# Kernel tuning notes

Measured on AMD Instinct MI355X. Metric: run time of the kernel, lower is better.

## Reference

```python
import jax, jax.numpy as jnp
import numpy as np

B, T, C, H = 4, 2048, 1024, 16
D = C // H  # head dim = 64

def setup_inputs() -> dict:
    key = jax.random.key(0)
    k1, k2, k3 = jax.random.split(key, 3)
    s = 1.0 / np.sqrt(C)
    return {
        "x": jax.random.normal(k1, (B, T, C), dtype=jnp.float32),
        "W_attn": jax.random.normal(k2, (C, 3 * C), dtype=jnp.float32) * s,
        "b_attn": jnp.zeros((3 * C,), dtype=jnp.float32),
        "W_proj": jax.random.normal(k3, (C, C), dtype=jnp.float32) * s,
        "b_proj": jnp.zeros((C,), dtype=jnp.float32),
    }

def reference(x, W_attn, b_attn, W_proj, b_proj):
    qkv = x @ W_attn + b_attn                      # [B,T,3C]
    q, k, v = jnp.split(qkv, 3, axis=-1)
    # [B,T,C] -> [B,H,T,D]
    q = q.reshape(B, T, H, D).transpose(0, 2, 1, 3)
    k = k.reshape(B, T, H, D).transpose(0, 2, 1, 3)
    v = v.reshape(B, T, H, D).transpose(0, 2, 1, 3)
    scale = 1.0 / np.sqrt(D)
    att = jnp.einsum('bhqd,bhkd->bhqk', q, k) * scale   # [B,H,T,T]
    causal = jnp.tril(jnp.ones((T, T), dtype=bool))
    att = jnp.where(causal[None, None], att, jnp.float32(-jnp.inf))
    att = jax.nn.softmax(att, axis=-1)
    y = jnp.einsum('bhqk,bhkd->bhqd', att, v)            # [B,H,T,D]
    y = y.transpose(0, 2, 1, 3).reshape(B, T, C)
    return y @ W_proj + b_proj
```

## Files before the change

kernel.cpp:

```cpp
#include <hip/hip_runtime.h>
#include <cstdint>
#include <cstddef>

typedef __bf16 bf16;
typedef __bf16 bf16x8 __attribute__((ext_vector_type(8)));
typedef __bf16 bf16x4 __attribute__((ext_vector_type(4)));
typedef short  s16x4  __attribute__((ext_vector_type(4)));
typedef float  f32x4  __attribute__((ext_vector_type(4)));

#define MFMA16(a, b, c) __builtin_amdgcn_mfma_f32_16x16x32_bf16((a), (b), (c), 0, 0, 0)

#if __has_builtin(__builtin_amdgcn_mfma_f32_16x16x16bf16_1k)
#define HAVE_K16 1
#else
#define HAVE_K16 0
#endif

#if __has_builtin(__builtin_amdgcn_exp2f)
#define EXP2(x) __builtin_amdgcn_exp2f(x)
#else
#define EXP2(x) exp2f(x)
#endif

constexpr int Bsz = 4;
constexpr int T   = 2048;
constexpr int Cd  = 1024;
constexpr int Hn  = 16;
constexpr int Mrows = Bsz * T;
constexpr int QKV_LD = 3 * Cd;

constexpr float QSCALE = 0.125f * 1.4426950408889634f;

__global__ __launch_bounds__(256) void prep(const float* __restrict__ x,
                                            const float* __restrict__ W_attn,
                                            const float* __restrict__ W_proj,
                                            bf16* __restrict__ xb,
                                            bf16* __restrict__ Wat,
                                            bf16* __restrict__ Wpt) {
    __shared__ float tile[32][33];
    const int bid = blockIdx.x;
    const int tid = threadIdx.x;
    if (bid < 4096) {
        const int i = (bid * 256 + tid) * 8;
        float4 a = *(const float4*)(x + i);
        float4 b = *(const float4*)(x + i + 4);
        bf16x8 o;
        o[0] = (bf16)a.x; o[1] = (bf16)a.y; o[2] = (bf16)a.z; o[3] = (bf16)a.w;
        o[4] = (bf16)b.x; o[5] = (bf16)b.y; o[6] = (bf16)b.z; o[7] = (bf16)b.w;
        *(bf16x8*)(xb + i) = o;
        return;
    }
    const float* W; bf16* Wt; int NDIM, bx, by;
    if (bid < 4096 + 3072) {
        const int r = bid - 4096;
        W = W_attn; Wt = Wat; NDIM = QKV_LD; bx = r % 96; by = r / 96;
    } else {
        const int r = bid - 7168;
        W = W_proj; Wt = Wpt; NDIM = Cd; bx = r & 31; by = r >> 5;
    }
    const int k0 = by * 32, n0 = bx * 32;
    const int tx = tid & 31, ty = tid >> 5;
    #pragma unroll
    for (int r = 0; r < 32; r += 8)
        tile[r + ty][tx] = W[(size_t)(k0 + r + ty) * NDIM + n0 + tx];
    __syncthreads();
    #pragma unroll
    for (int r = 0; r < 32; r += 8)
        Wt[(size_t)(n0 + r + ty) * Cd + k0 + tx] = (bf16)tile[tx][r + ty];
}

template <int N, bool OUT_BF16>
__global__ __launch_bounds__(512, 1) void gemm128x256(const bf16* __restrict__ A,
                                                      const bf16* __restrict__ Bt,
                                                      const float* __restrict__ bias,
                                                      void* __restrict__ outp,
                                                      float oscale, int oscale_n) {
    constexpr int K  = 1024;
    constexpr int KT = 16;
    __shared__ __align__(16) bf16 lds[73728];

    const int tid  = threadIdx.x;
    const int wv   = tid >> 6;
    const int lane = tid & 63;
    const int wm   = wv >> 2;
    const int wn   = wv & 3;
    const int quad = lane >> 4, c16 = lane & 15;
    const int sw   = c16 & 7;

    const int lin  = (int)blockIdx.x;
    const int mIdx = (lin & 7) + 8 * ((lin >> 3) & 7);
    const int nIdx = lin >> 6;
    const int m0   = mIdx * 128;
    const int n0   = nIdx * 256;

    auto stage = [&](int kt) {
        if (kt >= KT) return;
        const int db = kt % 3;
        #pragma unroll
        for (int r = 0; r < 2; ++r) {
            const int idx  = r * 512 + tid;
            const int slot = idx >> 3;
            const int kg   = kt * 64 + (((idx & 7) ^ (slot & 7)) << 3);
            __builtin_amdgcn_global_load_lds(
                (const __attribute__((address_space(1))) void*)(A + (size_t)(m0 + slot) * K + kg),
                (__attribute__((address_space(3))) void*)(&lds[db * 8192 + (r * 8 + wv) * 512]),
                16, 0, 0);
        }
        #pragma unroll
        for (int h = 0; h < 2; ++h)
            #pragma unroll
            for (int r = 0; r < 2; ++r) {
                const int idx  = r * 512 + tid;
                const int slot = idx >> 3;
                const int kg   = kt * 64 + (((idx & 7) ^ (slot & 7)) << 3);
                __builtin_amdgcn_global_load_lds(
                    (const __attribute__((address_space(1))) void*)(Bt + (size_t)(n0 + h * 128 + slot) * K + kg),
                    (__attribute__((address_space(3))) void*)(&lds[24576 + db * 16384 + h * 8192 + (r * 8 + wv) * 512]),
                    16, 0, 0);
            }
    };

    f32x4 acc[4][4] = {};
    bf16x8 af[4][2], bfv[4][2];

#define TILE_BODY(DB, SKT)                                                        \
    {                                                                             \
        _Pragma("unroll") for (int mq = 0; mq < 4; ++mq)                          \
            _Pragma("unroll") for (int ks = 0; ks < 2; ++ks)                      \
                af[mq][ks] = *(const bf16x8*)&lds[(DB) * 8192 +                   \
                    (wm * 64 + mq * 16 + c16) * 64 + (((ks * 4 + quad) ^ sw) << 3)]; \
        _Pragma("unroll") for (int nf = 0; nf < 4; ++nf)                          \
            _Pragma("unroll") for (int ks = 0; ks < 2; ++ks)                      \
                bfv[nf][ks] = *(const bf16x8*)&lds[24576 + (DB) * 16384 +         \
                    ((nf >> 1) * 128 + wn * 32 + (nf & 1) * 16 + c16) * 64 +      \
                    (((ks * 4 + quad) ^ sw) << 3)];                               \
        stage(SKT);                                                               \
        __builtin_amdgcn_s_setprio(1);                                            \
        _Pragma("unroll") for (int mq = 0; mq < 4; ++mq)                          \
            _Pragma("unroll") for (int nf = 0; nf < 4; ++nf)                      \
                _Pragma("unroll") for (int ks = 0; ks < 2; ++ks)                  \
                    acc[mq][nf] = MFMA16(af[mq][ks], bfv[nf][ks], acc[mq][nf]);   \
        __builtin_amdgcn_s_setprio(0);                                            \
    }
#define VMBAR(NSTR)                                                               \
    asm volatile("s_waitcnt vmcnt(" NSTR ")" ::: "memory");                       \
    __builtin_amdgcn_s_barrier();

    stage(0);
    stage(1);

    #pragma unroll 1
    for (int i = 0; i < 5; ++i) {
        const int u = 3 * i;
        VMBAR("6") TILE_BODY(0, u + 2)
        VMBAR("6") TILE_BODY(1, u + 3)
        VMBAR("6") TILE_BODY(2, u + 4)
    }
    VMBAR("0") TILE_BODY(0, KT)

#undef TILE_BODY
#undef VMBAR

    #pragma unroll
    for (int nf = 0; nf < 4; ++nf) {
        const int n = n0 + (nf >> 1) * 128 + wn * 32 + (nf & 1) * 16 + c16;
        const float bv = bias[n];
        const float sc = (n < oscale_n) ? oscale : 1.0f;
        #pragma unroll
        for (int mq = 0; mq < 4; ++mq) {
            const int rowb = m0 + wm * 64 + mq * 16 + quad * 4;
            #pragma unroll
            for (int r = 0; r < 4; ++r) {
                float val = (acc[mq][nf][r] + bv) * sc;
                if (OUT_BF16)
                    ((bf16*)outp)[(size_t)(rowb + r) * N + n] = (bf16)val;
                else
                    ((float*)outp)[(size_t)(rowb + r) * N + n] = val;
            }
        }
    }
}

__global__ __launch_bounds__(256, 2) void attn_fwd(const bf16* __restrict__ qkv,
                                                   bf16* __restrict__ yp0,
                                                   bf16* __restrict__ yp1,
                                                   bf16* __restrict__ yp2,
                                                   float* __restrict__ lp) {
    __shared__ __align__(16) bf16 Ks2[2][4096];
    __shared__ __align__(16) bf16 Vs[2][64 * 64];
#if !HAVE_K16
    __shared__ __align__(16) bf16 Ps[4][32 * 72];
#endif

    const int x    = blockIdx.x;
    const int xq   = x / 3;
    const int sgl  = x - 3 * xq;
    const int h    = blockIdx.y;
    const int bb   = blockIdx.z;
    const int tid  = threadIdx.x;
    const int w    = tid >> 6;
    const int lane = tid & 63;
    const int quad = lane >> 4, c16 = lane & 15;

    const size_t base = (size_t)(bb * T) * QKV_LD;

    const int g = tid >> 5;
    const int p = tid & 31;

    auto vs_store = [&](bf16* vbuf, const bf16x8& va, const bf16x8& vb) {
        #pragma unroll
        for (int j = 0; j < 8; ++j) {
            union { bf16 hh[2]; uint32_t u; } pk;
            pk.hh[0] = va[j]; pk.hh[1] = vb[j];
            const int row = 8 * g + j;
            *(uint32_t*)&vbuf[row * 64 + (((p >> 1) ^ (row & 15)) << 2) + ((p & 1) << 1)] = pk.u;
        }
    };

    bf16* __restrict__ ydst = (sgl == 0) ? yp0 : ((sgl == 1) ? yp1 : yp2);
    float* __restrict__ ldst = lp + (size_t)sgl * Mrows * Hn;

    for (int ph = 0; ph < 2; ++ph) {
        const int qt = ph ? xq : (15 - xq);
        const int q0 = qt * 128;
        const int rowbase = q0 + w * 32;

        const int n = 2 * qt + 2;
        int f0, f1;
        if (ph == 0) { f0 = (n + 2) / 3; f1 = (n + 1) / 3; }
        else         { f0 = n / 3;       f1 = (n + 1) / 3; }
        const int start = (sgl == 0) ? 0 : ((sgl == 1) ? f0 : f0 + f1);
        const int nkt   = (sgl == 0) ? f0 : ((sgl == 1) ? f1 : n - f0 - f1);

        __syncthreads();

        {
            const int kb = start * 64;
            #pragma unroll
            for (int ii = 0; ii < 2; ++ii) {
                const int i = 2 * w + ii;
                const bf16* gp = qkv + base + (size_t)(kb + 8 * i + (lane & 7)) * QKV_LD + Cd + h * 64 + (lane >> 3) * 8;
                __builtin_amdgcn_global_load_lds(
                    (const __attribute__((address_space(1))) void*)gp,
                    (__attribute__((address_space(3))) void*)(&Ks2[0][i * 512]), 16, 0, 0);
            }
            const bf16* vp = qkv + base + (size_t)(kb + 2 * p) * QKV_LD + 2 * Cd + h * 64 + g * 8;
            bf16x8 va = *(const bf16x8*)vp;
            bf16x8 vb = *(const bf16x8*)(vp + QKV_LD);
            vs_store(Vs[0], va, vb);
        }

        bf16x8 qf[2][2];
        #pragma unroll
        for (int mb = 0; mb < 2; ++mb) {
            const bf16* qp = qkv + base + (size_t)(rowbase + 16 * mb + c16) * QKV_LD + h * 64 + quad * 8;
            qf[mb][0] = *(const bf16x8*)qp;
            qf[mb][1] = *(const bf16x8*)(qp + 32);
        }

        f32x4 yacc[2][4] = {};
        float lsum[2] = {};

        for (int j = 0; j < nkt; ++j) {
            const int cur = j & 1, nxt = cur ^ 1;
            const int k0 = (start + j) * 64;
            __syncthreads();

            bf16x8 va, vb;
            const bool more = (j + 1 < nkt);
            if (more) {
                const int kn = k0 + 64;
                #pragma unroll
                for (int ii = 0; ii < 2; ++ii) {
                    const int i = 2 * w + ii;
                    const bf16* gp = qkv + base + (size_t)(kn + 8 * i + (lane & 7)) * QKV_LD + Cd + h * 64 + (lane >> 3) * 8;
                    __builtin_amdgcn_global_load_lds(
                        (const __attribute__((address_space(1))) void*)gp,
                        (__attribute__((address_space(3))) void*)(&Ks2[nxt][i * 512]), 16, 0, 0);
                }
                const bf16* vp = qkv + base + (size_t)(kn + 2 * p) * QKV_LD + 2 * Cd + h * 64 + g * 8;
                va = *(const bf16x8*)vp;
                vb = *(const bf16x8*)(vp + QKV_LD);
            }

            if (k0 <= rowbase + 31) {
                f32x4 s[2][4] = {};
                #pragma unroll
                for (int ks = 0; ks < 2; ++ks)
                    #pragma unroll
                    for (int blk = 0; blk < 4; ++blk) {
                        const bf16x8 kf = *(const bf16x8*)
                            &Ks2[cur][(2 * blk + (c16 >> 3)) * 512 + (4 * ks + quad) * 64 + (c16 & 7) * 8];
                        #pragma unroll
                        for (int mb = 0; mb < 2; ++mb)
                            s[mb][blk] = MFMA16(kf, qf[mb][ks], s[mb][blk]);
                    }

#if HAVE_K16
                union B4 { bf16x4 v; s16x4 s; } pb[2][4];
#endif
                #pragma unroll
                for (int mb = 0; mb < 2; ++mb) {
                    const int rb = rowbase + 16 * mb;
                    const int qglob = rb + c16;
                    const bool needMask = (k0 + 63 > rb);
                    #pragma unroll
                    for (int blk = 0; blk < 4; ++blk) {
                        #pragma unroll
                        for (int r = 0; r < 4; ++r) {
                            const int key = k0 + blk * 16 + quad * 4 + r;
                            float e = s[mb][blk][r];
                            if (needMask) e = (key > qglob) ? -INFINITY : e;
                            float pv = EXP2(e);
                            lsum[mb] += pv;
#if HAVE_K16
                            pb[mb][blk].v[r] = (bf16)pv;
#else
                            Ps[w][(mb * 16 + c16) * 72 + blk * 16 + quad * 4 + r] = (bf16)pv;
#endif
                        }
                    }
                }

#if HAVE_K16
                #pragma unroll
                for (int blk = 0; blk < 4; ++blk)
                    #pragma unroll
                    for (int d16 = 0; d16 < 4; ++d16) {
                        union B4u { bf16x4 v; s16x4 s; } vf;
                        vf.v = *(const bf16x4*)
                            &Vs[cur][(d16 * 16 + c16) * 64 + ((((blk << 2) | quad) ^ c16) << 2)];
                        #pragma unroll
                        for (int mb = 0; mb < 2; ++mb)
                            yacc[mb][d16] = __builtin_amdgcn_mfma_f32_16x16x16bf16_1k(
                                vf.s, pb[mb][blk].s, yacc[mb][d16], 0, 0, 0);
                    }
#else
                asm volatile("s_waitcnt lgkmcnt(0)" ::: "memory");
                #pragma unroll
                for (int ks = 0; ks < 2; ++ks) {
                    bf16x8 pf0 = *(const bf16x8*)&Ps[w][(0 * 16 + c16) * 72 + ks * 32 + quad * 8];
                    bf16x8 pf1 = *(const bf16x8*)&Ps[w][(1 * 16 + c16) * 72 + ks * 32 + quad * 8];
                    #pragma unroll
                    for (int d16 = 0; d16 < 4; ++d16) {
                        const int row = d16 * 16 + c16;
                        const int g0 = ks * 8 + quad * 2;
                        bf16x4 lo = *(const bf16x4*)&Vs[cur][row * 64 + ((g0 ^ c16) << 2)];
                        bf16x4 hi = *(const bf16x4*)&Vs[cur][row * 64 + (((g0 + 1) ^ c16) << 2)];
                        bf16x8 vfr;
                        vfr[0] = lo[0]; vfr[1] = lo[1]; vfr[2] = lo[2]; vfr[3] = lo[3];
                        vfr[4] = hi[0]; vfr[5] = hi[1]; vfr[6] = hi[2]; vfr[7] = hi[3];
                        yacc[0][d16] = MFMA16(pf0, vfr, yacc[0][d16]);
                        yacc[1][d16] = MFMA16(pf1, vfr, yacc[1][d16]);
                    }
                }
#endif
            }

            if (more)
                vs_store(Vs[nxt], va, vb);
        }

        #pragma unroll
        for (int mb = 0; mb < 2; ++mb) {
            lsum[mb] += __shfl_xor(lsum[mb], 16);
            lsum[mb] += __shfl_xor(lsum[mb], 32);
        }

#if HAVE_K16
        #pragma unroll
        for (int mb = 0; mb < 2; ++mb) {
            const int row = rowbase + 16 * mb + c16;
            bf16* yw = ydst + (size_t)(bb * T + row) * Cd + h * 64;
            #pragma unroll
            for (int d16 = 0; d16 < 4; ++d16) {
                bf16x4 o;
                #pragma unroll
                for (int r = 0; r < 4; ++r)
                    o[r] = (bf16)(yacc[mb][d16][r]);
                *(bf16x4*)(yw + d16 * 16 + quad * 4) = o;
            }
            if (quad == 0)
                ldst[(size_t)(bb * T + row) * Hn + h] = lsum[mb];
        }
#else
        #pragma unroll
        for (int mb = 0; mb < 2; ++mb)
            #pragma unroll
            for (int r = 0; r < 4; ++r) {
                const float lsv = __shfl(lsum[mb], quad * 4 + r);
                const int row = rowbase + 16 * mb + quad * 4 + r;
                bf16* yw = ydst + (size_t)(bb * T + row) * Cd + h * 64;
                #pragma unroll
                for (int d16 = 0; d16 < 4; ++d16)
                    yw[d16 * 16 + c16] = (bf16)(yacc[mb][d16][r]);
                if (c16 == 0)
                    ldst[(size_t)(bb * T + row) * Hn + h] = lsv;
            }
#endif
    }
}

__global__ __launch_bounds__(256) void attn_combine(const bf16* __restrict__ yp0,
                                                    const bf16* __restrict__ yp1,
                                                    const bf16* __restrict__ yp2,
                                                    const float* __restrict__ lp,
                                                    bf16* __restrict__ y) {
    int i = (blockIdx.x * 256 + threadIdx.x) * 8;
    int row = i >> 10;
    int hh  = (i & 1023) >> 6;
    const size_t S = (size_t)Mrows * Hn;
    const size_t li = (size_t)row * Hn + hh;
    float l = lp[li] + lp[S + li] + lp[2 * S + li];
    float inv = 1.f / l;
    bf16x8 a = *(const bf16x8*)(yp0 + i);
    bf16x8 b = *(const bf16x8*)(yp1 + i);
    bf16x8 c = *(const bf16x8*)(yp2 + i);
    bf16x8 o;
    #pragma unroll
    for (int j = 0; j < 8; ++j)
        o[j] = (bf16)(((float)a[j] + (float)b[j] + (float)c[j]) * inv);
    *(bf16x8*)(y + i) = o;
}

extern "C" void kernel_launch(void* const* d_in, const int* in_sizes, int n_in,
                              void* d_out, int out_size, void* d_ws, size_t ws_size,
                              hipStream_t stream) {
    const float* x      = (const float*)d_in[0];
    const float* W_attn = (const float*)d_in[1];
    const float* b_attn = (const float*)d_in[2];
    const float* W_proj = (const float*)d_in[3];
    const float* b_proj = (const float*)d_in[4];
    float* out = (float*)d_out;

    bf16* xb   = (bf16*)d_ws;
    bf16* Wat  = xb  + (size_t)Mrows * Cd;
    bf16* Wpt  = Wat + (size_t)QKV_LD * Cd;
    bf16* qkv  = Wpt + (size_t)Cd * Cd;
    bf16* yb   = qkv + (size_t)Mrows * QKV_LD;
    bf16* yp1  = yb  + (size_t)Mrows * Cd;
    bf16*  yp2 = xb;
    float* lp  = (float*)Wat;

    prep<<<8192, 256, 0, stream>>>(x, W_attn, W_proj, xb, Wat, Wpt);

    gemm128x256<QKV_LD, true><<<dim3((Mrows / 128) * (QKV_LD / 256)), dim3(512), 0, stream>>>(
        xb, Wat, b_attn, qkv, QSCALE, Cd);

    attn_fwd<<<dim3(24, Hn, Bsz), 256, 0, stream>>>(qkv, yb, yp1, yp2, lp);
    attn_combine<<<(Mrows * Cd) / (256 * 8), 256, 0, stream>>>(yb, yp1, yp2, lp, yb);

    gemm128x256<Cd, false><<<dim3((Mrows / 128) * (Cd / 256)), dim3(512), 0, stream>>>(
        yb, Wpt, b_proj, out, 1.0f, 0);
}
```

Measured before the change: 266.2 us.

## Software-pipeline QK^T one tile ahead with triple-buffered K in LDS

Triple-buffers the K tiles in shared memory and prefetches K two tiles ahead. The QK^T MFMAs for tile j+1 now run in the same iteration as the softmax and PV for tile j, so the exp and MFMA work can interleave and the load latency is hidden. This costs more LDS (an extra 8 KB K buffer) and extra registers for the next-score accumulators, which may reduce occupancy under launch_bounds(256,2). The barrier moves to the end of each iteration.

```diff
diff --git a/kernel.cpp b/kernel.cpp
--- a/kernel.cpp
+++ b/kernel.cpp
@@ -186,8 +186,8 @@
                                                    bf16* __restrict__ yp1,
                                                    bf16* __restrict__ yp2,
                                                    float* __restrict__ lp) {
-    __shared__ __align__(16) bf16 Ks2[2][4096];
-    __shared__ __align__(16) bf16 Vs[2][64 * 64];
+    __shared__ __align__(16) bf16 Ks3[3][4096];
+    __shared__ __align__(16) bf16 Vs[2][4096];
 #if !HAVE_K16
     __shared__ __align__(16) bf16 Ps[4][32 * 72];
 #endif
@@ -216,6 +216,16 @@
             *(uint32_t*)&vbuf[row * 64 + (((p >> 1) ^ (row & 15)) << 2) + ((p & 1) << 1)] = pk.u;
         }
     };
+    auto k_stage = [&](int buf, int kb) {
+        #pragma unroll
+        for (int ii = 0; ii < 2; ++ii) {
+            const int i = 2 * w + ii;
+            const bf16* gp = qkv + base + (size_t)(kb + 8 * i + (lane & 7)) * QKV_LD + Cd + h * 64 + (lane >> 3) * 8;
+            __builtin_amdgcn_global_load_lds(
+                (const __attribute__((address_space(1))) void*)gp,
+                (__attribute__((address_space(3))) void*)(&Ks3[buf][i * 512]), 16, 0, 0);
+        }
+    };
 
     bf16* __restrict__ ydst = (sgl == 0) ? yp0 : ((sgl == 1) ? yp1 : yp2);
     float* __restrict__ ldst = lp + (size_t)sgl * Mrows * Hn;
@@ -236,14 +246,8 @@
 
         {
             const int kb = start * 64;
-            #pragma unroll
-            for (int ii = 0; ii < 2; ++ii) {
-                const int i = 2 * w + ii;
-                const bf16* gp = qkv + base + (size_t)(kb + 8 * i + (lane & 7)) * QKV_LD + Cd + h * 64 + (lane >> 3) * 8;
-                __builtin_amdgcn_global_load_lds(
-                    (const __attribute__((address_space(1))) void*)gp,
-                    (__attribute__((address_space(3))) void*)(&Ks2[0][i * 512]), 16, 0, 0);
-            }
+            k_stage(0, kb);
+            if (nkt >= 2) k_stage(1, kb + 64);
             const bf16* vp = qkv + base + (size_t)(kb + 2 * p) * QKV_LD + 2 * Cd + h * 64 + g * 8;
             bf16x8 va = *(const bf16x8*)vp;
             bf16x8 vb = *(const bf16x8*)(vp + QKV_LD);
@@ -260,42 +264,53 @@
 
         f32x4 yacc[2][4] = {};
         float lsum[2] = {};
+        f32x4 scur[2][4] = {};
+
+        __syncthreads();
+
+        if (nkt > 0 && start * 64 <= rowbase + 31) {
+            #pragma unroll
+            for (int ks = 0; ks < 2; ++ks)
+                #pragma unroll
+                for (int blk = 0; blk < 4; ++blk) {
+                    const bf16x8 kf = *(const bf16x8*)
+                        &Ks3[0][(2 * blk + (c16 >> 3)) * 512 + (4 * ks + quad) * 64 + (c16 & 7) * 8];
+                    #pragma unroll
+                    for (int mb = 0; mb < 2; ++mb)
+                        scur[mb][blk] = MFMA16(kf, qf[mb][ks], scur[mb][blk]);
+                }
+        }
 
         for (int j = 0; j < nkt; ++j) {
-            const int cur = j & 1, nxt = cur ^ 1;
             const int k0 = (start + j) * 64;
-            __syncthreads();
-
+            const int k0n = k0 + 64;
+            const bool more = (j + 1 < nkt);
+
+            if (j + 2 < nkt)
+                k_stage((j + 2) % 3, k0 + 128);
             bf16x8 va, vb;
-            const bool more = (j + 1 < nkt);
             if (more) {
-                const int kn = k0 + 64;
-                #pragma unroll
-                for (int ii = 0; ii < 2; ++ii) {
-                    const int i = 2 * w + ii;
-                    const bf16* gp = qkv + base + (size_t)(kn + 8 * i + (lane & 7)) * QKV_LD + Cd + h * 64 + (lane >> 3) * 8;
-                    __builtin_amdgcn_global_load_lds(
-                        (const __attribute__((address_space(1))) void*)gp,
-                        (__attribute__((address_space(3))) void*)(&Ks2[nxt][i * 512]), 16, 0, 0);
-                }
-                const bf16* vp = qkv + base + (size_t)(kn + 2 * p) * QKV_LD + 2 * Cd + h * 64 + g * 8;
+                const bf16* vp = qkv + base + (size_t)(k0n + 2 * p) * QKV_LD + 2 * Cd + h * 64 + g * 8;
                 va = *(const bf16x8*)vp;
                 vb = *(const bf16x8*)(vp + QKV_LD);
             }
 
-            if (k0 <= rowbase + 31) {
-                f32x4 s[2][4] = {};
+            f32x4 snxt[2][4] = {};
+            if (more && k0n <= rowbase + 31) {
+                const bf16* kbuf = Ks3[(j + 1) % 3];
                 #pragma unroll
                 for (int ks = 0; ks < 2; ++ks)
                     #pragma unroll
                     for (int blk = 0; blk < 4; ++blk) {
                         const bf16x8 kf = *(const bf16x8*)
-                            &Ks2[cur][(2 * blk + (c16 >> 3)) * 512 + (4 * ks + quad) * 64 + (c16 & 7) * 8];
+                            &kbuf[(2 * blk + (c16 >> 3)) * 512 + (4 * ks + quad) * 64 + (c16 & 7) * 8];
                         #pragma unroll
                         for (int mb = 0; mb < 2; ++mb)
-                            s[mb][blk] = MFMA16(kf, qf[mb][ks], s[mb][blk]);
+                            snxt[mb][blk] = MFMA16(kf, qf[mb][ks], snxt[mb][blk]);
                     }
-
+            }
+
+            if (k0 <= rowbase + 31) {
 #if HAVE_K16
                 union B4 { bf16x4 v; s16x4 s; } pb[2][4];
 #endif
@@ -309,7 +324,7 @@
                         #pragma unroll
                         for (int r = 0; r < 4; ++r) {
                             const int key = k0 + blk * 16 + quad * 4 + r;
-                            float e = s[mb][blk][r];
+                            float e = scur[mb][blk][r];
                             if (needMask) e = (key > qglob) ? -INFINITY : e;
                             float pv = EXP2(e);
                             lsum[mb] += pv;
@@ -323,13 +338,14 @@
                 }
 
 #if HAVE_K16
+                const bf16* vbuf = Vs[j & 1];
                 #pragma unroll
                 for (int blk = 0; blk < 4; ++blk)
                     #pragma unroll
                     for (int d16 = 0; d16 < 4; ++d16) {
                         union B4u { bf16x4 v; s16x4 s; } vf;
                         vf.v = *(const bf16x4*)
-                            &Vs[cur][(d16 * 16 + c16) * 64 + ((((blk << 2) | quad) ^ c16) << 2)];
+                            &vbuf[(d16 * 16 + c16) * 64 + ((((blk << 2) | quad) ^ c16) << 2)];
                         #pragma unroll
                         for (int mb = 0; mb < 2; ++mb)
                             yacc[mb][d16] = __builtin_amdgcn_mfma_f32_16x16x16bf16_1k(
@@ -337,6 +353,7 @@
                     }
 #else
                 asm volatile("s_waitcnt lgkmcnt(0)" ::: "memory");
+                const bf16* vbuf = Vs[j & 1];
                 #pragma unroll
                 for (int ks = 0; ks < 2; ++ks) {
                     bf16x8 pf0 = *(const bf16x8*)&Ps[w][(0 * 16 + c16) * 72 + ks * 32 + quad * 8];
@@ -345,8 +362,8 @@
                     for (int d16 = 0; d16 < 4; ++d16) {
                         const int row = d16 * 16 + c16;
                         const int g0 = ks * 8 + quad * 2;
-                        bf16x4 lo = *(const bf16x4*)&Vs[cur][row * 64 + ((g0 ^ c16) << 2)];
-                        bf16x4 hi = *(const bf16x4*)&Vs[cur][row * 64 + (((g0 + 1) ^ c16) << 2)];
+                        bf16x4 lo = *(const bf16x4*)&vbuf[row * 64 + ((g0 ^ c16) << 2)];
+                        bf16x4 hi = *(const bf16x4*)&vbuf[row * 64 + (((g0 + 1) ^ c16) << 2)];
                         bf16x8 vfr;
                         vfr[0] = lo[0]; vfr[1] = lo[1]; vfr[2] = lo[2]; vfr[3] = lo[3];
                         vfr[4] = hi[0]; vfr[5] = hi[1]; vfr[6] = hi[2]; vfr[7] = hi[3];
@@ -358,7 +375,15 @@
             }
 
             if (more)
-                vs_store(Vs[nxt], va, vb);
+                vs_store(Vs[(j + 1) & 1], va, vb);
+
+            __syncthreads();
+
+            #pragma unroll
+            for (int mb = 0; mb < 2; ++mb)
+                #pragma unroll
+                for (int blk = 0; blk < 4; ++blk)
+                    scur[mb][blk] = snxt[mb][blk];
         }
 
         #pragma unroll
```

Measured after the change: 271.1 us. No clear change (+1.9%).
